# Optimization experiments

Hardware: AMD Instinct MI355X
Metric: run time of the kernel (lower is better)

The kernel has to match this reference:

```python
import jax, jax.numpy as jnp
import numpy as np

PATCHSIZE = 512
SLACK = 64  # max(inputsize // 8, 32)


def make_grid(H, W, patchsize, slack):
    # numpy replica of grid_for_patches (static shapes at trace time)
    step = patchsize - slack
    gy = np.minimum(np.arange(patchsize, H + step, step), H)
    gx = np.minimum(np.arange(patchsize, W + step, step), W)
    yy, xx = np.meshgrid(gy, gx, indexing='ij')
    g = np.stack([yy, xx], axis=-1)                      # (gh, gw, 2) bottom-right corners
    grid = np.concatenate([g - patchsize, g], axis=-1)   # (gh, gw, 4) = (y0, x0, y1, x1)
    return np.maximum(grid, 0)


def paste_coords(grid, H, W, slack, i):
    # numpy replica of paste_patch coordinate math; i is a Python int
    gh, gw = grid.shape[0], grid.shape[1]
    hs = slack // 2
    lh = (grid[gh - 2, gw - 2, 2:4] - grid[gh - 1, gw - 1, 0:2]) // 2
    crop_top = np.concatenate([[0], np.full(gh - 2, hs), [lh[0]]])
    crop_left = np.concatenate([[0], np.full(gw - 2, hs), [lh[1]]])
    crop_bottom = np.concatenate([np.full(gh - 1, -hs), [H]])
    crop_right = np.concatenate([np.full(gw - 1, -hs), [W]])
    d0 = np.stack(np.meshgrid(crop_top, crop_left, indexing='ij'), axis=-1)
    d1 = np.stack(np.meshgrid(crop_bottom, crop_right, indexing='ij'), axis=-1)
    d = np.concatenate([d0, d1], axis=-1)                # (gh, gw, 4)
    di = d.reshape(-1, 4)[i]
    gi = (grid + d).reshape(-1, 4)[i]
    return [int(v) for v in di], [int(v) for v in gi]


def setup_inputs() -> dict:
    key = jax.random.key(0)
    k1, k2, k3, k4 = jax.random.split(key, 4)
    H = Wd = 4096
    x_u8 = jax.random.randint(k1, (1, H, Wd, 3), 0, 256, dtype=jnp.int32)
    y = jax.random.normal(k2, (1, 1, H, Wd), dtype=jnp.float32)
    W = jax.random.normal(k3, (1, 3, 3, 3), dtype=jnp.float32) * 0.1
    b = jax.random.normal(k4, (1,), dtype=jnp.float32) * 0.1
    return {'x_u8': x_u8, 'y': y, 'W': W, 'b': b, 'i': 40}


def reference(x_u8, y, W, b, i):
    # x_u8: (B,H,W,3) int -> BCHW float in [0,1]
    x = jnp.transpose(x_u8.astype(jnp.float32) / 255.0, (0, 3, 1, 2))
    H, Wd = x.shape[2], x.shape[3]
    grid = make_grid(H, Wd, PATCHSIZE, SLACK)
    p = grid.reshape(-1, 4)[i]  # (y0, x0, y1, x1), Python ints
    xp = x[..., int(p[0]):int(p[2]), int(p[1]):int(p[3])]  # (B,3,512,512)
    # stand-in for the UNet: single 3x3 conv, 1 output channel, + sigmoid
    yp = jax.lax.conv_general_dilated(
        xp, W, window_strides=(1, 1), padding='SAME',
        dimension_numbers=('NCHW', 'OIHW', 'NCHW')) + b[None, :, None, None]
    yp = jax.nn.sigmoid(yp)
    # maybe_new_y
    y0 = y if i > 0 else jnp.zeros((x.shape[0], 1, H, Wd), jnp.float32)
    # paste_patch
    di, gi = paste_coords(grid, H, Wd, SLACK, i)
    y_out = y0.at[..., gi[0]:gi[2], gi[1]:gi[3]].set(yp[..., di[0]:di[2], di[1]:di[3]])
    return y_out
```

## Files before the change

### kernel.cpp

```cpp
#include <hip/hip_runtime.h>
#include <math.h>

#define PATCH 512
#define SLACK 64
#define STEP  (PATCH - SLACK)
#define HS    (SLACK / 2)

struct Geom {
    int p0, p1;
    int gi0, gi1;
    int ph, pw;
};

__device__ __forceinline__ Geom compute_geom(int i, int H, int W) {
    const int gh = (H - PATCH + STEP - 1) / STEP + 1;
    const int gw = (W - PATCH + STEP - 1) / STEP + 1;
    const int r = (unsigned)i / (unsigned)gw;
    const int c = (unsigned)i % (unsigned)gw;
    const int gyr = min(PATCH + r * STEP, H);
    const int gxc = min(PATCH + c * STEP, W);
    Geom g;
    g.p0 = max(gyr - PATCH, 0);
    g.p1 = max(gxc - PATCH, 0);
    const int gy_m2 = min(PATCH + (gh - 2) * STEP, H);
    const int gx_m2 = min(PATCH + (gw - 2) * STEP, W);
    const int gy_m1 = min(PATCH + (gh - 1) * STEP, H);
    const int gx_m1 = min(PATCH + (gw - 1) * STEP, W);
    const int lh0 = (gy_m2 - (gy_m1 - PATCH)) / 2;
    const int lh1 = (gx_m2 - (gx_m1 - PATCH)) / 2;
    const int di0 = (r == 0) ? 0 : ((r == gh - 1) ? lh0 : HS);
    const int di1 = (c == 0) ? 0 : ((c == gw - 1) ? lh1 : HS);
    const int di2 = (r < gh - 1) ? (PATCH - HS) : PATCH;
    const int di3 = (c < gw - 1) ? (PATCH - HS) : PATCH;
    g.gi0 = g.p0 + di0;
    g.gi1 = g.p1 + di1;
    g.ph  = di2 - di0;
    g.pw  = di3 - di1;
    return g;
}

__device__ __forceinline__ float conv_px(const int* __restrict__ x,
                                         const float* __restrict__ Wt,
                                         float bias, int py, int px,
                                         int p0, int p1, int W) {
    const float inv255 = 1.0f / 255.0f;
    float acc = bias;
#pragma unroll
    for (int ky = 0; ky < 3; ++ky) {
        const int ppy = py + ky - 1;
        if (ppy < 0 || ppy >= PATCH) continue;
        const int ih = p0 + ppy;
#pragma unroll
        for (int kx = 0; kx < 3; ++kx) {
            const int ppx = px + kx - 1;
            if (ppx < 0 || ppx >= PATCH) continue;
            const int iw = p1 + ppx;
            const int* __restrict__ xp = x + ((size_t)ih * W + iw) * 3;
            acc += Wt[0 * 9 + ky * 3 + kx] * ((float)xp[0] * inv255)
                 + Wt[1 * 9 + ky * 3 + kx] * ((float)xp[1] * inv255)
                 + Wt[2 * 9 + ky * 3 + kx] * ((float)xp[2] * inv255);
        }
    }
    return 1.0f / (1.0f + expf(-acc));
}

__global__ __launch_bounds__(256) void fused_kernel(
        const int* __restrict__ x, const float* __restrict__ y,
        const float* __restrict__ Wt, const float* __restrict__ bp,
        const int* __restrict__ ip, float* __restrict__ out,
        int H, int W) {
    const int row = blockIdx.x;
    const int t = threadIdx.x;
    const int i = __builtin_amdgcn_readfirstlane(ip[0]);
    const Geom g = compute_geom(i, H, W);
    const int w4 = W >> 2;
    const size_t rowbase = (size_t)row * w4;
    const float4* __restrict__ y4 = (const float4*)y;
    float4* __restrict__ o4 = (float4*)out;

    const bool rowin = (row >= g.gi0) && (row < g.gi0 + g.ph);
    if (!rowin) {
        if (i > 0) {
            for (int q = t; q < w4; q += 256)
                o4[rowbase + q] = y4[rowbase + q];
        } else {
            const float4 z = make_float4(0.f, 0.f, 0.f, 0.f);
            for (int q = t; q < w4; q += 256)
                o4[rowbase + q] = z;
        }
        return;
    }

    const float bias = bp[0];
    const int cl = g.gi1, cr = g.gi1 + g.pw;
    for (int q = t; q < w4; q += 256) {
        const int c0 = q << 2;
        float4 v;
        if (c0 + 3 < cl || c0 >= cr) {
            v = (i > 0) ? y4[rowbase + q] : make_float4(0.f, 0.f, 0.f, 0.f);
        } else {
            float vv[4];
#pragma unroll
            for (int j = 0; j < 4; ++j) {
                const int col = c0 + j;
                if (col >= cl && col < cr) {
                    vv[j] = conv_px(x, Wt, bias, row - g.p0, col - g.p1,
                                    g.p0, g.p1, W);
                } else {
                    vv[j] = (i > 0) ? y[(size_t)row * W + col] : 0.f;
                }
            }
            v = make_float4(vv[0], vv[1], vv[2], vv[3]);
        }
        o4[rowbase + q] = v;
    }
}

extern "C" void kernel_launch(void* const* d_in, const int* in_sizes, int n_in,
                              void* d_out, int out_size, void* d_ws, size_t ws_size,
                              hipStream_t stream) {
    const int*   x  = (const int*)d_in[0];
    const float* y  = (const float*)d_in[1];
    const float* Wt = (const float*)d_in[2];
    const float* b  = (const float*)d_in[3];
    const int*   ip = (const int*)d_in[4];
    float* out = (float*)d_out;

    int H = 1;
    while ((long long)(H + 1) * (H + 1) <= (long long)out_size) ++H;
    const int Wd = H;

    fused_kernel<<<dim3(H), dim3(256), 0, stream>>>(x, y, Wt, b, ip, out, H, Wd);
}
```

Baseline: 31.71 us.

## Split work into flat copy blocks and separate per-pixel conv blocks

Replaces the one-block-per-row kernel with a flat grid: copy blocks each handle 256 float4s of the output and skip columns inside the patch, and extra blocks each compute 256 patch pixels of the convolution, one pixel per thread. This spreads the conv work across many blocks instead of serializing it over the few rows that intersect the patch, which should reduce load imbalance. It relies on W being a power of two and divisible by 1024 for the shift/mask indexing, and conv writes become scalar stores.

```diff
diff --git a/kernel.cpp b/kernel.cpp
--- a/kernel.cpp
+++ b/kernel.cpp
@@ -5,6 +5,8 @@
 #define SLACK 64
 #define STEP  (PATCH - SLACK)
 #define HS    (SLACK / 2)
+
+typedef float f32x4 __attribute__((ext_vector_type(4)));
 
 struct Geom {
     int p0, p1;
@@ -64,56 +66,64 @@
     return 1.0f / (1.0f + expf(-acc));
 }
 
-__global__ __launch_bounds__(256) void fused_kernel(
+__global__ __launch_bounds__(256) void fused_one(
         const int* __restrict__ x, const float* __restrict__ y,
         const float* __restrict__ Wt, const float* __restrict__ bp,
         const int* __restrict__ ip, float* __restrict__ out,
-        int H, int W) {
-    const int row = blockIdx.x;
-    const int t = threadIdx.x;
+        int H, int W, int CB) {
     const int i = __builtin_amdgcn_readfirstlane(ip[0]);
     const Geom g = compute_geom(i, H, W);
+    const int b = blockIdx.x;
+    const int t = threadIdx.x;
     const int w4 = W >> 2;
-    const size_t rowbase = (size_t)row * w4;
-    const float4* __restrict__ y4 = (const float4*)y;
-    float4* __restrict__ o4 = (float4*)out;
 
-    const bool rowin = (row >= g.gi0) && (row < g.gi0 + g.ph);
-    if (!rowin) {
-        if (i > 0) {
-            for (int q = t; q < w4; q += 256)
-                o4[rowbase + q] = y4[rowbase + q];
+    if (b < CB) {
+        const int q = b * 256 + t;
+        const int sh = 31 - __clz(w4);
+        const int row = q >> sh;
+        const int c0 = (q & (w4 - 1)) << 2;
+        const f32x4* __restrict__ y4 = (const f32x4*)y;
+        f32x4* __restrict__ o4 = (f32x4*)out;
+
+        const bool rowin = (row >= g.gi0) && (row < g.gi0 + g.ph);
+        const int cl = g.gi1, cr = g.gi1 + g.pw;
+        const int bc0 = ((b * 256) & (w4 - 1)) << 2;
+        if (!rowin || (bc0 + 1023 < cl) || (bc0 >= cr)) {
+            f32x4 v;
+            if (i > 0) v = y4[q];
+            else       v = (f32x4){0.f, 0.f, 0.f, 0.f};
+            o4[q] = v;
         } else {
-            const float4 z = make_float4(0.f, 0.f, 0.f, 0.f);
-            for (int q = t; q < w4; q += 256)
-                o4[rowbase + q] = z;
+            if (c0 + 3 < cl || c0 >= cr) {
+                f32x4 v;
+                if (i > 0) v = y4[q];
+                else       v = (f32x4){0.f, 0.f, 0.f, 0.f};
+                o4[q] = v;
+            } else if (c0 >= cl && c0 + 3 < cr) {
+            } else {
+#pragma unroll
+                for (int j = 0; j < 4; ++j) {
+                    const int col = c0 + j;
+                    if (col < cl || col >= cr) {
+                        out[(size_t)row * W + col] =
+                            (i > 0) ? y[(size_t)row * W + col] : 0.f;
+                    }
+                }
+            }
         }
         return;
     }
 
+    const int p = (b - CB) * 256 + t;
+    const int np = g.ph * g.pw;
+    if (p >= np) return;
+    const int pr = (unsigned)p / (unsigned)g.pw;
+    const int pc = (unsigned)p % (unsigned)g.pw;
     const float bias = bp[0];
-    const int cl = g.gi1, cr = g.gi1 + g.pw;
-    for (int q = t; q < w4; q += 256) {
-        const int c0 = q << 2;
-        float4 v;
-        if (c0 + 3 < cl || c0 >= cr) {
-            v = (i > 0) ? y4[rowbase + q] : make_float4(0.f, 0.f, 0.f, 0.f);
-        } else {
-            float vv[4];
-#pragma unroll
-            for (int j = 0; j < 4; ++j) {
-                const int col = c0 + j;
-                if (col >= cl && col < cr) {
-                    vv[j] = conv_px(x, Wt, bias, row - g.p0, col - g.p1,
-                                    g.p0, g.p1, W);
-                } else {
-                    vv[j] = (i > 0) ? y[(size_t)row * W + col] : 0.f;
-                }
-            }
-            v = make_float4(vv[0], vv[1], vv[2], vv[3]);
-        }
-        o4[rowbase + q] = v;
-    }
+    const float v = conv_px(x, Wt, bias,
+                            (g.gi0 - g.p0) + pr, (g.gi1 - g.p1) + pc,
+                            g.p0, g.p1, W);
+    out[(size_t)(g.gi0 + pr) * W + (g.gi1 + pc)] = v;
 }
 
 extern "C" void kernel_launch(void* const* d_in, const int* in_sizes, int n_in,
@@ -130,5 +140,8 @@
     while ((long long)(H + 1) * (H + 1) <= (long long)out_size) ++H;
     const int Wd = H;
 
-    fused_kernel<<<dim3(H), dim3(256), 0, stream>>>(x, y, Wt, b, ip, out, H, Wd);
+    const int CB = (H * (Wd >> 2)) / 256;
+    const int CONVB = (PATCH * PATCH) / 256;
+    fused_one<<<dim3(CB + CONVB), dim3(256), 0, stream>>>(
+        x, y, Wt, b, ip, out, H, Wd, CB);
 }
```

New measurement: 28.30 us. 1.12x faster.
